# Kernel tuning notes

Hardware: AMD Instinct MI355X
Metric: run time of the kernel (lower is better)

Reference implementation:

```python
import jax, jax.numpy as jnp
import numpy as np

B, C, H, W = 16, 128, 48, 48
C4 = C // 4
N = H * W
BN_EPS = 1e-5


def conv_bn_relu(x, w, gamma, beta, mean, var):
    # 1x1 conv (no bias) as channel contraction, then eval-mode BatchNorm, then ReLU
    y = jnp.einsum('bchw,oc->bohw', x, w)
    scale = gamma / jnp.sqrt(var + BN_EPS)
    y = y * scale[None, :, None, None] + (beta - mean * scale)[None, :, None, None]
    return jax.nn.relu(y)


def setup_inputs() -> dict:
    key = jax.random.key(0)
    ks = jax.random.split(key, 16)
    inp = {
        'x_en': jax.random.normal(ks[0], (B, C, H, W), dtype=jnp.float32),
        'x_de': jax.random.normal(ks[1], (B, C, H, W), dtype=jnp.float32),
        'x_cat': jax.random.normal(ks[2], (B, 2 * C, H, W), dtype=jnp.float32),
        # Get_KQ: Conv2d(C -> C/4, 1x1, no bias) + BN(C/4) (shared for K and Q)
        'w_kq': jax.random.normal(ks[3], (C4, C), dtype=jnp.float32) * 0.05,
        'kq_gamma': jax.random.normal(ks[4], (C4,), dtype=jnp.float32) * 0.1 + 1.0,
        'kq_beta': jax.random.normal(ks[5], (C4,), dtype=jnp.float32) * 0.1,
        'kq_mean': jax.random.normal(ks[6], (C4,), dtype=jnp.float32) * 0.1,
        'kq_var': jax.random.uniform(ks[7], (C4,), dtype=jnp.float32) + 0.5,
        # Get_V: Conv2d(C -> C, 1x1, no bias) + BN(C)
        'w_v': jax.random.normal(ks[8], (C, C), dtype=jnp.float32) * 0.05,
        'v_gamma': jax.random.normal(ks[9], (C,), dtype=jnp.float32) * 0.1 + 1.0,
        'v_beta': jax.random.normal(ks[10], (C,), dtype=jnp.float32) * 0.1,
        'v_mean': jax.random.normal(ks[11], (C,), dtype=jnp.float32) * 0.1,
        'v_var': jax.random.uniform(ks[12], (C,), dtype=jnp.float32) + 0.5,
        # reduce_channels: Conv2d(2C -> C, 1x1, no bias) + BN(C)
        'w_red': jax.random.normal(ks[13], (C, 2 * C), dtype=jnp.float32) * 0.05,
        'red_gamma': jax.random.normal(ks[14], (C,), dtype=jnp.float32) * 0.1 + 1.0,
        'red_beta': jax.random.normal(ks[15], (C,), dtype=jnp.float32) * 0.1,
        'red_mean': jax.random.normal(jax.random.fold_in(key, 100), (C,), dtype=jnp.float32) * 0.1,
        'red_var': jax.random.uniform(jax.random.fold_in(key, 101), (C,), dtype=jnp.float32) + 0.5,
    }
    return inp


def reference(x_en, x_de, x_cat,
              w_kq, kq_gamma, kq_beta, kq_mean, kq_var,
              w_v, v_gamma, v_beta, v_mean, v_var,
              w_red, red_gamma, red_beta, red_mean, red_var):
    Kf = conv_bn_relu(x_en, w_kq, kq_gamma, kq_beta, kq_mean, kq_var).reshape(B, C4, N)
    Qf = conv_bn_relu(x_de, w_kq, kq_gamma, kq_beta, kq_mean, kq_var).reshape(B, C4, N)
    # KQ[b, n, m] = sum_k K[b, k, n] * Q[b, k, m]  -> [B, N, N]
    KQ = jnp.einsum('bkn,bkm->bnm', Kf, Qf)
    # GLOBAL softmax over the flattened N*N map (per batch), not per row
    A = jax.nn.softmax(KQ.reshape(B, N * N), axis=1).reshape(B, N, N)
    x = conv_bn_relu(x_cat, w_red, red_gamma, red_beta, red_mean, red_var)
    V = conv_bn_relu(x, w_v, v_gamma, v_beta, v_mean, v_var).reshape(B, C, N)
    # FeatureMap[b, c, n] = sum_m V[b, c, m] * A[b, n, m]
    feat = jnp.einsum('bcm,bnm->bcn', V, A).reshape(B, C, H, W)
    return jnp.concatenate([x, feat], axis=1)
```

## Files before the change

### kernel.cpp

```cpp
#include <hip/hip_runtime.h>
#include <math.h>

#define C    128
#define C4   32
#define NN   2304
#define BN_EPS 1e-5f
#define NEG_INF -3.402823466e38f
#define LOG2E 1.4426950408889634f

typedef short bf16x8 __attribute__((ext_vector_type(8)));
typedef float f32x4 __attribute__((ext_vector_type(4)));

#define SOFT_BARRIER() asm volatile("s_waitcnt lgkmcnt(0)\n\ts_barrier" ::: "memory")

__device__ inline unsigned short f2bf(float f) {
    unsigned int u = __float_as_uint(f);
    u += 0x7fffu + ((u >> 16) & 1u);
    return (unsigned short)(u >> 16);
}

__device__ inline unsigned int pk2bf(float a, float b) {
#if __has_builtin(__builtin_amdgcn_cvt_pk_bf16_f32)
    typedef __bf16 bf2 __attribute__((ext_vector_type(2)));
    bf2 v = __builtin_amdgcn_cvt_pk_bf16_f32(a, b);
    return __builtin_bit_cast(unsigned int, v);
#else
    unsigned int ua = __float_as_uint(a); ua += 0x7fffu + ((ua >> 16) & 1u);
    unsigned int ub = __float_as_uint(b); ub += 0x7fffu + ((ub >> 16) & 1u);
    return __builtin_amdgcn_perm(ub, ua, 0x07060302u);
#endif
}

__device__ inline float fexp2(float x) {
#if __has_builtin(__builtin_amdgcn_exp2f)
    return __builtin_amdgcn_exp2f(x);
#else
    return __expf(x * 0.69314718055994531f);
#endif
}


__global__ __launch_bounds__(256) void k_wprep(
    const float* __restrict__ wkq, const float* __restrict__ kq_g,
    const float* __restrict__ kq_b, const float* __restrict__ kq_m,
    const float* __restrict__ kq_v,
    const float* __restrict__ wv, const float* __restrict__ v_g,
    const float* __restrict__ v_b, const float* __restrict__ v_m,
    const float* __restrict__ v_v,
    const float* __restrict__ wred, const float* __restrict__ red_g,
    const float* __restrict__ red_b, const float* __restrict__ red_m,
    const float* __restrict__ red_v,
    unsigned short* __restrict__ wkq_bf, unsigned short* __restrict__ wv_bf,
    unsigned short* __restrict__ wred_bf,
    float* __restrict__ kq_sh, float* __restrict__ v_sh, float* __restrict__ red_sh)
{
    const int t = blockIdx.x * 256 + threadIdx.x;
    if (t < 4096) {
        const int o = t >> 7;
        const float sc = kq_g[o] * rsqrtf(kq_v[o] + BN_EPS);
        wkq_bf[t] = f2bf(wkq[t] * sc);
        if ((t & 127) == 0) kq_sh[o] = kq_b[o] - kq_m[o] * sc;
    } else if (t < 4096 + 16384) {
        const int e = t - 4096;
        const int o = e >> 7;
        const float sc = v_g[o] * rsqrtf(v_v[o] + BN_EPS);
        wv_bf[e] = f2bf(wv[e] * sc);
        if ((e & 127) == 0) v_sh[o] = v_b[o] - v_m[o] * sc;
    } else if (t < 4096 + 16384 + 32768) {
        const int e = t - 20480;
        const int o = e >> 8;
        const float sc = red_g[o] * rsqrtf(red_v[o] + BN_EPS);
        wred_bf[e] = f2bf(wred[e] * sc);
        if ((e & 255) == 0) red_sh[o] = red_b[o] - red_m[o] * sc;
    }
}

__global__ __launch_bounds__(256) void k_kqredv(
    const float* __restrict__ x0, const float* __restrict__ x1,
    const float* __restrict__ xcat,
    const unsigned short* __restrict__ wbf, const float* __restrict__ shift,
    unsigned short* __restrict__ Kt, unsigned short* __restrict__ Qt,
    const unsigned short* __restrict__ wred_bf, const float* __restrict__ red_sh,
    const unsigned short* __restrict__ wv_bf,  const float* __restrict__ v_sh,
    float* __restrict__ out, unsigned short* __restrict__ Vf)
{
    __shared__ __align__(16) unsigned char smem[20608];
    const int wg = blockIdx.x;
    const int tid = threadIdx.x;
    const int w = tid >> 6, lane = tid & 63;
    const int quad = lane >> 4, l16 = lane & 15;
    const int cp = tid >> 4;
    const int g  = tid & 15;

    if (wg < 768) {
        typedef unsigned short XsT[48][40];
        XsT* Xs = (XsT*)smem;
        unsigned int* Xv = (unsigned int*)(smem + 7680);

        const int b = wg / 48, n0 = (wg % 48) * 48;
        const float* xin = xcat + (size_t)b * 2 * C * NN;

        f32x4 acc[2][3];
#pragma unroll
        for (int mt = 0; mt < 2; mt++)
#pragma unroll
            for (int nt = 0; nt < 3; nt++) acc[mt][nt] = (f32x4){0.f, 0.f, 0.f, 0.f};

        float av[3], bv[3];
        {
            const float* xr = xin + (size_t)(2 * cp) * NN + n0 + g;
#pragma unroll
            for (int j = 0; j < 3; j++) { av[j] = xr[j * 16]; bv[j] = xr[NN + j * 16]; }
        }

        for (int k = 0; k < 8; ++k) {
            unsigned int uu[3];
#pragma unroll
            for (int j = 0; j < 3; j++) uu[j] = pk2bf(av[j], bv[j]);
            if (k < 7) {
                const float* xr = xin + (size_t)((k + 1) * 32 + 2 * cp) * NN + n0 + g;
#pragma unroll
                for (int j = 0; j < 3; j++) { av[j] = xr[j * 16]; bv[j] = xr[NN + j * 16]; }
            }
            unsigned int* Xw = (unsigned int*)Xs[k & 1];
#pragma unroll
            for (int j = 0; j < 3; j++)
                Xw[(j * 16 + g) * 20 + cp] = uu[j];
            SOFT_BARRIER();
            bf16x8 af[2];
#pragma unroll
            for (int mt = 0; mt < 2; mt++)
                af[mt] = *(const bf16x8*)&wred_bf[(size_t)(w * 32 + mt * 16 + l16) * (2 * C) + k * 32 + quad * 8];
#pragma unroll
            for (int nt = 0; nt < 3; nt++) {
                const bf16x8 bfr = *(const bf16x8*)&Xs[k & 1][nt * 16 + l16][quad * 8];
#pragma unroll
                for (int mt = 0; mt < 2; mt++)
                    acc[mt][nt] = __builtin_amdgcn_mfma_f32_16x16x32_bf16(af[mt], bfr, acc[mt][nt], 0, 0, 0);
            }
        }

        {
            float* ob = out + (size_t)b * (2 * C * NN);
#pragma unroll
            for (int mt = 0; mt < 2; mt++) {
                float sh[4];
#pragma unroll
                for (int r = 0; r < 4; r++) sh[r] = red_sh[w * 32 + mt * 16 + quad * 4 + r];
#pragma unroll
                for (int nt = 0; nt < 3; nt++) {
                    const int n = n0 + nt * 16 + l16;
                    float v[4];
#pragma unroll
                    for (int r = 0; r < 4; r++) {
                        const int o = w * 32 + mt * 16 + quad * 4 + r;
                        v[r] = fmaxf(acc[mt][nt][r] + sh[r], 0.f);
                        ob[(size_t)o * NN + n] = v[r];
                    }
                    const int op0 = 16 * w + mt * 8 + quad * 2;
                    Xv[(op0 + 0) * 49 + nt * 16 + l16] = pk2bf(v[0], v[1]);
                    Xv[(op0 + 1) * 49 + nt * 16 + l16] = pk2bf(v[2], v[3]);
                }
            }
        }
        SOFT_BARRIER();

        f32x4 vacc[2][3];
#pragma unroll
        for (int mt = 0; mt < 2; mt++)
#pragma unroll
            for (int nt = 0; nt < 3; nt++) vacc[mt][nt] = (f32x4){0.f, 0.f, 0.f, 0.f};

        for (int c0 = 0; c0 < C; c0 += 32) {
            bf16x8 af[2];
#pragma unroll
            for (int mt = 0; mt < 2; mt++)
                af[mt] = *(const bf16x8*)&wv_bf[(size_t)(w * 32 + mt * 16 + l16) * C + c0 + quad * 8];
#pragma unroll
            for (int nt = 0; nt < 3; nt++) {
                const int col = nt * 16 + l16;
                const int cp0 = c0 / 2 + quad * 4;
                uint4 u;
                u.x = Xv[(cp0 + 0) * 49 + col];
                u.y = Xv[(cp0 + 1) * 49 + col];
                u.z = Xv[(cp0 + 2) * 49 + col];
                u.w = Xv[(cp0 + 3) * 49 + col];
                const bf16x8 bfr = __builtin_bit_cast(bf16x8, u);
#pragma unroll
                for (int mt = 0; mt < 2; mt++)
                    vacc[mt][nt] = __builtin_amdgcn_mfma_f32_16x16x32_bf16(af[mt], bfr, vacc[mt][nt], 0, 0, 0);
            }
        }

#pragma unroll
        for (int mt = 0; mt < 2; mt++) {
            float sh[4];
#pragma unroll
            for (int r = 0; r < 4; r++) sh[r] = v_sh[w * 32 + mt * 16 + quad * 4 + r];
#pragma unroll
            for (int nt = 0; nt < 3; nt++)
#pragma unroll
                for (int r = 0; r < 4; r++) {
                    const int o = w * 32 + mt * 16 + quad * 4 + r;
                    const int n = n0 + nt * 16 + l16;
                    Vf[(((size_t)b * 72 + (n >> 5)) * 128 + o) * 32 + (n & 31)] =
                        f2bf(fmaxf(vacc[mt][nt][r] + sh[r], 0.f));
                }
        }
    } else {
        typedef unsigned short Xs2T[128][40];
        Xs2T* Xs = (Xs2T*)smem;

        const int e = wg - 768;
        const int z = e / 288;
        const int rem = e - z * 288;
        const int b = rem / 18, n0 = (rem % 18) * 128;
        const int nbase = w * 32;

        const float* xin = (z ? x1 : x0) + (size_t)b * C * NN;

        f32x4 acc[2][2];
#pragma unroll
        for (int mt = 0; mt < 2; mt++)
#pragma unroll
            for (int nt = 0; nt < 2; nt++) acc[mt][nt] = (f32x4){0.f, 0.f, 0.f, 0.f};

        float av[8], bv[8];
        {
            const float* xr = xin + (size_t)(2 * cp) * NN + n0 + g;
#pragma unroll
            for (int j = 0; j < 8; j++) { av[j] = xr[j * 16]; bv[j] = xr[NN + j * 16]; }
        }

        for (int k = 0; k < 4; ++k) {
            unsigned int uu[8];
#pragma unroll
            for (int j = 0; j < 8; j++) uu[j] = pk2bf(av[j], bv[j]);
            if (k < 3) {
                const float* xr = xin + (size_t)((k + 1) * 32 + 2 * cp) * NN + n0 + g;
#pragma unroll
                for (int j = 0; j < 8; j++) { av[j] = xr[j * 16]; bv[j] = xr[NN + j * 16]; }
            }
            unsigned int* Xw = (unsigned int*)Xs[k & 1];
#pragma unroll
            for (int j = 0; j < 8; j++)
                Xw[(j * 16 + g) * 20 + cp] = uu[j];
            SOFT_BARRIER();
            bf16x8 af[2];
#pragma unroll
            for (int mt = 0; mt < 2; mt++)
                af[mt] = *(const bf16x8*)&wbf[(size_t)(mt * 16 + l16) * C + k * 32 + quad * 8];
#pragma unroll
            for (int nt = 0; nt < 2; nt++) {
                const bf16x8 bfr = *(const bf16x8*)&Xs[k & 1][nbase + nt * 16 + l16][quad * 8];
#pragma unroll
                for (int mt = 0; mt < 2; mt++)
                    acc[mt][nt] = __builtin_amdgcn_mfma_f32_16x16x32_bf16(af[mt], bfr, acc[mt][nt], 0, 0, 0);
            }
        }

        unsigned short* ob16 = z ? Qt : Kt;
        const float osc = z ? 1.f : LOG2E;
#pragma unroll
        for (int mt = 0; mt < 2; mt++)
#pragma unroll
            for (int nt = 0; nt < 2; nt++)
#pragma unroll
                for (int r = 0; r < 4; r++) {
                    const int o = mt * 16 + quad * 4 + r;
                    const int n = n0 + nbase + nt * 16 + l16;
                    const float sh = shift[o];
                    ob16[((size_t)b * NN + n) * 32 + o] =
                        f2bf(fmaxf(acc[mt][nt][r] + sh, 0.f) * osc);
                }
    }
}

__global__ __launch_bounds__(256) void k_stats(
    const unsigned short* __restrict__ Kt, const unsigned short* __restrict__ Qt,
    float* __restrict__ bmax, float* __restrict__ bsum)
{
    const int tid = threadIdx.x;
    const int w = tid >> 6, lane = tid & 63;
    const int quad = lane >> 4, l16 = lane & 15;
    const int wg = blockIdx.x;
    const int xcd = wg & 7;
    const int slot = wg >> 3;
    const int b = xcd * 2 + slot / 324;
    const int tile = slot % 324;
    const int my = tile / 18, mx = tile % 18;
    const int n0 = mx * 128, m0 = my * 128;
    const unsigned short* Kb = Kt + (size_t)b * NN * 32;
    const unsigned short* Qb = Qt + (size_t)b * NN * 32;

    bf16x8 kf[8], qf[2];
#pragma unroll
    for (int nt = 0; nt < 8; nt++)
        kf[nt] = *(const bf16x8*)&Kb[(size_t)(n0 + nt * 16 + l16) * 32 + quad * 8];
#pragma unroll
    for (int mt = 0; mt < 2; mt++)
        qf[mt] = *(const bf16x8*)&Qb[(size_t)(m0 + w * 32 + mt * 16 + l16) * 32 + quad * 8];

    f32x4 s[16];
#pragma unroll
    for (int mt = 0; mt < 2; mt++)
#pragma unroll
        for (int nt = 0; nt < 8; nt++) {
            f32x4 z = (f32x4){0.f, 0.f, 0.f, 0.f};
            s[mt * 8 + nt] = __builtin_amdgcn_mfma_f32_16x16x32_bf16(qf[mt], kf[nt], z, 0, 0, 0);
        }

    float lmax = NEG_INF;
#pragma unroll
    for (int i = 0; i < 16; i++)
        lmax = fmaxf(lmax, fmaxf(fmaxf(s[i][0], s[i][1]), fmaxf(s[i][2], s[i][3])));
    float lsum = 0.f;
#pragma unroll
    for (int i = 0; i < 16; i++)
        lsum += fexp2(s[i][0] - lmax) + fexp2(s[i][1] - lmax) +
                fexp2(s[i][2] - lmax) + fexp2(s[i][3] - lmax);

#pragma unroll
    for (int off = 32; off > 0; off >>= 1) {
        const float omax = __shfl_xor(lmax, off);
        const float osum = __shfl_xor(lsum, off);
        const float nmax = fmaxf(lmax, omax);
        lsum = lsum * fexp2(lmax - nmax) + osum * fexp2(omax - nmax);
        lmax = nmax;
    }
    __shared__ float smax[4], ssum[4];
    if (lane == 0) { smax[w] = lmax; ssum[w] = lsum; }
    __syncthreads();
    if (tid == 0) {
        float M = smax[0], S = ssum[0];
        for (int i = 1; i < 4; i++) {
            const float nmax = fmaxf(M, smax[i]);
            S = S * fexp2(M - nmax) + ssum[i] * fexp2(smax[i] - nmax);
            M = nmax;
        }
        const int idx = (b * 18 + my) * 18 + mx;
        bmax[idx] = M;
        bsum[idx] = S;
    }
}

__global__ __launch_bounds__(256) void k_fin(
    const float* __restrict__ bmax, const float* __restrict__ bsum,
    float* __restrict__ Ms, float* __restrict__ Sinv)
{
    __shared__ float rmax[256], rsum[256];
    const int b = blockIdx.x, tid = threadIdx.x;
    float lmax = NEG_INF, lsum = 0.f;
    for (int i = tid; i < 324; i += 256) {
        const float m = bmax[b * 324 + i], s = bsum[b * 324 + i];
        const float nmax = fmaxf(lmax, m);
        lsum = lsum * fexp2(lmax - nmax) + s * fexp2(m - nmax);
        lmax = nmax;
    }
    rmax[tid] = lmax; rsum[tid] = lsum;
    __syncthreads();
    for (int st = 128; st > 0; st >>= 1) {
        if (tid < st) {
            const float m2 = rmax[tid + st], s2 = rsum[tid + st];
            const float nmax = fmaxf(rmax[tid], m2);
            rsum[tid] = rsum[tid] * fexp2(rmax[tid] - nmax) + s2 * fexp2(m2 - nmax);
            rmax[tid] = nmax;
        }
        __syncthreads();
    }
    if (tid == 0) { Ms[b] = rmax[0]; Sinv[b] = 1.f / rsum[0]; }
}

__global__ __launch_bounds__(256) void k_feat(
    const unsigned short* __restrict__ Kt, const unsigned short* __restrict__ Qt,
    const unsigned short* __restrict__ Vf, const float* __restrict__ Ms,
    const float* __restrict__ Sinv, float* __restrict__ out)
{
    __shared__ __align__(16) unsigned short Et[2][48][136];
    const int tid = threadIdx.x;
    const int w = tid >> 6, lane = tid & 63;
    const int quad = lane >> 4, l16 = lane & 15;
    const int wg = blockIdx.x;
    const int xcd = wg & 7;
    const int slot = wg >> 3;
    const int b = xcd * 2 + slot / 48;
    const int n0 = (slot % 48) * 48;
    const unsigned short* Kb = Kt + (size_t)b * NN * 32;
    const unsigned short* Qb = Qt + (size_t)b * NN * 32;
    const unsigned short* Vb = Vf + (size_t)b * 72 * 128 * 32;
    const float M = Ms[b], Si = Sinv[b];

    bf16x8 kf[3];
#pragma unroll
    for (int nt = 0; nt < 3; nt++)
        kf[nt] = *(const bf16x8*)&Kb[(size_t)(n0 + nt * 16 + l16) * 32 + quad * 8];

    f32x4 acc[2][3];
#pragma unroll
    for (int i = 0; i < 2; i++)
#pragma unroll
        for (int j = 0; j < 3; j++) acc[i][j] = (f32x4){0.f, 0.f, 0.f, 0.f};

    {
        const bf16x8 q00 = *(const bf16x8*)&Qb[(size_t)(w * 32 + l16) * 32 + quad * 8];
        const bf16x8 q01 = *(const bf16x8*)&Qb[(size_t)(w * 32 + 16 + l16) * 32 + quad * 8];
        f32x4 s0[3], s1[3];
#pragma unroll
        for (int nt = 0; nt < 3; nt++) {
            f32x4 z = (f32x4){0.f, 0.f, 0.f, 0.f};
            s0[nt] = __builtin_amdgcn_mfma_f32_16x16x32_bf16(q00, kf[nt], z, 0, 0, 0);
            s1[nt] = __builtin_amdgcn_mfma_f32_16x16x32_bf16(q01, kf[nt], z, 0, 0, 0);
        }
#pragma unroll
        for (int nt = 0; nt < 3; nt++) {
            const unsigned int a0 = pk2bf(fexp2(s0[nt][0] - M), fexp2(s0[nt][1] - M));
            const unsigned int a1 = pk2bf(fexp2(s0[nt][2] - M), fexp2(s0[nt][3] - M));
            *(uint2*)&Et[0][nt * 16 + l16][w * 32 + quad * 4] = make_uint2(a0, a1);
            const unsigned int b0 = pk2bf(fexp2(s1[nt][0] - M), fexp2(s1[nt][1] - M));
            const unsigned int b1 = pk2bf(fexp2(s1[nt][2] - M), fexp2(s1[nt][3] - M));
            *(uint2*)&Et[0][nt * 16 + l16][w * 32 + 16 + quad * 4] = make_uint2(b0, b1);
        }
    }
    bf16x8 qc0 = *(const bf16x8*)&Qb[(size_t)(128 + w * 32 + l16) * 32 + quad * 8];
    bf16x8 qc1 = *(const bf16x8*)&Qb[(size_t)(128 + w * 32 + 16 + l16) * 32 + quad * 8];
    SOFT_BARRIER();

    for (int k = 0; k < 18; ++k) {
        const int cur = k & 1;
        const int mt0 = k * 4;
        const int mq = (k + 2 < 18 ? k + 2 : 0) * 128;
        bf16x8 qn0 = *(const bf16x8*)&Qb[(size_t)(mq + w * 32 + l16) * 32 + quad * 8];
        bf16x8 qn1 = *(const bf16x8*)&Qb[(size_t)(mq + w * 32 + 16 + l16) * 32 + quad * 8];
        bf16x8 vc[2][4];
#pragma unroll
        for (int ct = 0; ct < 2; ct++)
#pragma unroll
            for (int ks = 0; ks < 4; ks++)
                vc[ct][ks] = *(const bf16x8*)&Vb[(((size_t)(mt0 + ks)) * 128 + w * 32 + ct * 16 + l16) * 32 + quad * 8];

        if (k < 17) {
            f32x4 s0[3], s1[3];
#pragma unroll
            for (int nt = 0; nt < 3; nt++) {
                f32x4 z = (f32x4){0.f, 0.f, 0.f, 0.f};
                s0[nt] = __builtin_amdgcn_mfma_f32_16x16x32_bf16(qc0, kf[nt], z, 0, 0, 0);
                s1[nt] = __builtin_amdgcn_mfma_f32_16x16x32_bf16(qc1, kf[nt], z, 0, 0, 0);
            }
#pragma unroll
            for (int nt = 0; nt < 3; nt++) {
                const unsigned int a0 = pk2bf(fexp2(s0[nt][0] - M), fexp2(s0[nt][1] - M));
                const unsigned int a1 = pk2bf(fexp2(s0[nt][2] - M), fexp2(s0[nt][3] - M));
                *(uint2*)&Et[cur ^ 1][nt * 16 + l16][w * 32 + quad * 4] = make_uint2(a0, a1);
                const unsigned int b0 = pk2bf(fexp2(s1[nt][0] - M), fexp2(s1[nt][1] - M));
                const unsigned int b1 = pk2bf(fexp2(s1[nt][2] - M), fexp2(s1[nt][3] - M));
                *(uint2*)&Et[cur ^ 1][nt * 16 + l16][w * 32 + 16 + quad * 4] = make_uint2(b0, b1);
            }
        }

        __builtin_amdgcn_s_setprio(1);
#pragma unroll
        for (int ks = 0; ks < 4; ks++) {
#pragma unroll
            for (int nt = 0; nt < 3; nt++) {
                const bf16x8 ef = *(const bf16x8*)&Et[cur][nt * 16 + l16][ks * 32 + quad * 8];
                acc[0][nt] = __builtin_amdgcn_mfma_f32_16x16x32_bf16(vc[0][ks], ef, acc[0][nt], 0, 0, 0);
                acc[1][nt] = __builtin_amdgcn_mfma_f32_16x16x32_bf16(vc[1][ks], ef, acc[1][nt], 0, 0, 0);
            }
        }
        __builtin_amdgcn_s_setprio(0);
        SOFT_BARRIER();
        qc0 = qn0;
        qc1 = qn1;
    }

    float* ob = out + (size_t)b * 2 * C * NN + (size_t)C * NN + n0;
#pragma unroll
    for (int ct = 0; ct < 2; ct++)
#pragma unroll
        for (int nt = 0; nt < 3; nt++)
#pragma unroll
            for (int r = 0; r < 4; r++) {
                const int c = w * 32 + ct * 16 + quad * 4 + r;
                ob[(size_t)c * NN + nt * 16 + l16] = acc[ct][nt][r] * Si;
            }
}

extern "C" void kernel_launch(void* const* d_in, const int* in_sizes, int n_in,
                              void* d_out, int out_size, void* d_ws, size_t ws_size,
                              hipStream_t stream)
{
    const float* x_en   = (const float*)d_in[0];
    const float* x_de   = (const float*)d_in[1];
    const float* x_cat  = (const float*)d_in[2];
    const float* w_kq   = (const float*)d_in[3];
    const float* kq_g   = (const float*)d_in[4];
    const float* kq_b   = (const float*)d_in[5];
    const float* kq_m   = (const float*)d_in[6];
    const float* kq_v   = (const float*)d_in[7];
    const float* w_v    = (const float*)d_in[8];
    const float* v_g    = (const float*)d_in[9];
    const float* v_b    = (const float*)d_in[10];
    const float* v_m    = (const float*)d_in[11];
    const float* v_v    = (const float*)d_in[12];
    const float* w_red  = (const float*)d_in[13];
    const float* red_g  = (const float*)d_in[14];
    const float* red_b  = (const float*)d_in[15];
    const float* red_m  = (const float*)d_in[16];
    const float* red_v  = (const float*)d_in[17];

    unsigned short* Kt      = (unsigned short*)d_ws;
    unsigned short* Qt      = Kt + 1179648;
    unsigned short* Vf      = Qt + 1179648;
    unsigned short* wkq_bf  = Vf + 4718592;
    unsigned short* wv_bf   = wkq_bf + 4096;
    unsigned short* wred_bf = wv_bf + 16384;
    float* bmax = (float*)(wred_bf + 32768);
    float* bsum = bmax + 16 * 324;
    float* Ms   = bsum + 16 * 324;
    float* Sinv = Ms + 16;
    float* kq_sh  = Sinv + 16;
    float* v_sh   = kq_sh + 32;
    float* red_sh = v_sh + 128;
    float* out  = (float*)d_out;

    k_wprep<<<208, 256, 0, stream>>>(
        w_kq, kq_g, kq_b, kq_m, kq_v,
        w_v, v_g, v_b, v_m, v_v,
        w_red, red_g, red_b, red_m, red_v,
        wkq_bf, wv_bf, wred_bf, kq_sh, v_sh, red_sh);

    k_kqredv<<<1344, 256, 0, stream>>>(
        x_en, x_de, x_cat, wkq_bf, kq_sh, Kt, Qt,
        wred_bf, red_sh, wv_bf, v_sh, out, Vf);

    k_stats<<<5184, 256, 0, stream>>>(Kt, Qt, bmax, bsum);
    k_fin  <<<16, 256, 0, stream>>>(bmax, bsum, Ms, Sinv);
    k_feat <<<768, 256, 0, stream>>>(Kt, Qt, Vf, Ms, Sinv, out);
}
```

Measured before the change: 220.1 us.

## Fuse softmax final reduction into feat kernel and swizzle LDS tile

Removes the separate k_fin launch. Each k_feat block now recomputes the per-batch global max and sum from the 324 partial stats itself, which trades one kernel launch and its dependency gap for some redundant reduction work in every block. The padded LDS tile for the exponentiated scores is replaced by an unpadded tile with an XOR swizzle on 16-byte chunks, meant to avoid bank conflicts while using less shared memory. The max and sum reductions in k_stats are rewritten as trees with multiple accumulators to shorten dependency chains.

```diff
diff --git a/kernel.cpp b/kernel.cpp
--- a/kernel.cpp
+++ b/kernel.cpp
@@ -310,26 +310,37 @@
             s[mt * 8 + nt] = __builtin_amdgcn_mfma_f32_16x16x32_bf16(qf[mt], kf[nt], z, 0, 0, 0);
         }
 
-    float lmax = NEG_INF;
+    float v[16];
 #pragma unroll
     for (int i = 0; i < 16; i++)
-        lmax = fmaxf(lmax, fmaxf(fmaxf(s[i][0], s[i][1]), fmaxf(s[i][2], s[i][3])));
-    float lsum = 0.f;
-#pragma unroll
-    for (int i = 0; i < 16; i++)
-        lsum += fexp2(s[i][0] - lmax) + fexp2(s[i][1] - lmax) +
-                fexp2(s[i][2] - lmax) + fexp2(s[i][3] - lmax);
+        v[i] = fmaxf(fmaxf(s[i][0], s[i][1]), fmaxf(s[i][2], s[i][3]));
+#pragma unroll
+    for (int st = 8; st > 0; st >>= 1)
+#pragma unroll
+        for (int i = 0; i < st; i++) v[i] = fmaxf(v[i], v[i + st]);
+    const float lmax = v[0];
+
+    float l0 = 0.f, l1 = 0.f, l2 = 0.f, l3 = 0.f;
+#pragma unroll
+    for (int i = 0; i < 16; i += 4) {
+        l0 += fexp2(s[i+0][0] - lmax) + fexp2(s[i+0][1] - lmax) + fexp2(s[i+0][2] - lmax) + fexp2(s[i+0][3] - lmax);
+        l1 += fexp2(s[i+1][0] - lmax) + fexp2(s[i+1][1] - lmax) + fexp2(s[i+1][2] - lmax) + fexp2(s[i+1][3] - lmax);
+        l2 += fexp2(s[i+2][0] - lmax) + fexp2(s[i+2][1] - lmax) + fexp2(s[i+2][2] - lmax) + fexp2(s[i+2][3] - lmax);
+        l3 += fexp2(s[i+3][0] - lmax) + fexp2(s[i+3][1] - lmax) + fexp2(s[i+3][2] - lmax) + fexp2(s[i+3][3] - lmax);
+    }
+    float lsum = (l0 + l1) + (l2 + l3);
+    float lm = lmax;
 
 #pragma unroll
     for (int off = 32; off > 0; off >>= 1) {
-        const float omax = __shfl_xor(lmax, off);
+        const float omax = __shfl_xor(lm, off);
         const float osum = __shfl_xor(lsum, off);
-        const float nmax = fmaxf(lmax, omax);
-        lsum = lsum * fexp2(lmax - nmax) + osum * fexp2(omax - nmax);
-        lmax = nmax;
+        const float nmax = fmaxf(lm, omax);
+        lsum = lsum * fexp2(lm - nmax) + osum * fexp2(omax - nmax);
+        lm = nmax;
     }
     __shared__ float smax[4], ssum[4];
-    if (lane == 0) { smax[w] = lmax; ssum[w] = lsum; }
+    if (lane == 0) { smax[w] = lm; ssum[w] = lsum; }
     __syncthreads();
     if (tid == 0) {
         float M = smax[0], S = ssum[0];
@@ -344,39 +355,14 @@
     }
 }
 
-__global__ __launch_bounds__(256) void k_fin(
-    const float* __restrict__ bmax, const float* __restrict__ bsum,
-    float* __restrict__ Ms, float* __restrict__ Sinv)
-{
-    __shared__ float rmax[256], rsum[256];
-    const int b = blockIdx.x, tid = threadIdx.x;
-    float lmax = NEG_INF, lsum = 0.f;
-    for (int i = tid; i < 324; i += 256) {
-        const float m = bmax[b * 324 + i], s = bsum[b * 324 + i];
-        const float nmax = fmaxf(lmax, m);
-        lsum = lsum * fexp2(lmax - nmax) + s * fexp2(m - nmax);
-        lmax = nmax;
-    }
-    rmax[tid] = lmax; rsum[tid] = lsum;
-    __syncthreads();
-    for (int st = 128; st > 0; st >>= 1) {
-        if (tid < st) {
-            const float m2 = rmax[tid + st], s2 = rsum[tid + st];
-            const float nmax = fmaxf(rmax[tid], m2);
-            rsum[tid] = rsum[tid] * fexp2(rmax[tid] - nmax) + s2 * fexp2(m2 - nmax);
-            rmax[tid] = nmax;
-        }
-        __syncthreads();
-    }
-    if (tid == 0) { Ms[b] = rmax[0]; Sinv[b] = 1.f / rsum[0]; }
-}
-
 __global__ __launch_bounds__(256) void k_feat(
     const unsigned short* __restrict__ Kt, const unsigned short* __restrict__ Qt,
-    const unsigned short* __restrict__ Vf, const float* __restrict__ Ms,
-    const float* __restrict__ Sinv, float* __restrict__ out)
+    const unsigned short* __restrict__ Vf,
+    const float* __restrict__ bmax, const float* __restrict__ bsum,
+    float* __restrict__ out)
 {
-    __shared__ __align__(16) unsigned short Et[2][48][136];
+    __shared__ __align__(16) unsigned short Et[2][48][128];
+    __shared__ float2 redw[4];
     const int tid = threadIdx.x;
     const int w = tid >> 6, lane = tid & 63;
     const int quad = lane >> 4, l16 = lane & 15;
@@ -388,7 +374,43 @@
     const unsigned short* Kb = Kt + (size_t)b * NN * 32;
     const unsigned short* Qb = Qt + (size_t)b * NN * 32;
     const unsigned short* Vb = Vf + (size_t)b * 72 * 128 * 32;
-    const float M = Ms[b], Si = Sinv[b];
+
+    float M, Si;
+    {
+        float lm = NEG_INF, ls = 0.f;
+        for (int i = tid; i < 324; i += 256) {
+            const float m = bmax[b * 324 + i], s = bsum[b * 324 + i];
+            const float nm = fmaxf(lm, m);
+            ls = ls * fexp2(lm - nm) + s * fexp2(m - nm);
+            lm = nm;
+        }
+#pragma unroll
+        for (int off = 32; off > 0; off >>= 1) {
+            const float om = __shfl_xor(lm, off);
+            const float os = __shfl_xor(ls, off);
+            const float nm = fmaxf(lm, om);
+            ls = ls * fexp2(lm - nm) + os * fexp2(om - nm);
+            lm = nm;
+        }
+        if (lane == 0) redw[w] = make_float2(lm, ls);
+        __syncthreads();
+        float Mm = redw[0].x, Ss = redw[0].y;
+#pragma unroll
+        for (int i = 1; i < 4; i++) {
+            const float m2 = redw[i].x, s2 = redw[i].y;
+            const float nm = fmaxf(Mm, m2);
+            Ss = Ss * fexp2(Mm - nm) + s2 * fexp2(m2 - nm);
+            Mm = nm;
+        }
+        M = Mm;
+        Si = 1.f / Ss;
+    }
+
+    const int aswz = l16 & 7;
+    const int wby0 = 64 * w + 8 * quad;
+    const int wof0 = ((((wby0 >> 4) ^ aswz) << 4) | (wby0 & 15));
+    const int wby1 = wby0 + 32;
+    const int wof1 = ((((wby1 >> 4) ^ aswz) << 4) | (wby1 & 15));
 
     bf16x8 kf[3];
 #pragma unroll
@@ -413,12 +435,13 @@
         }
 #pragma unroll
         for (int nt = 0; nt < 3; nt++) {
+            char* rowp = (char*)&Et[0][nt * 16 + l16][0];
             const unsigned int a0 = pk2bf(fexp2(s0[nt][0] - M), fexp2(s0[nt][1] - M));
             const unsigned int a1 = pk2bf(fexp2(s0[nt][2] - M), fexp2(s0[nt][3] - M));
-            *(uint2*)&Et[0][nt * 16 + l16][w * 32 + quad * 4] = make_uint2(a0, a1);
+            *(uint2*)(rowp + wof0) = make_uint2(a0, a1);
             const unsigned int b0 = pk2bf(fexp2(s1[nt][0] - M), fexp2(s1[nt][1] - M));
             const unsigned int b1 = pk2bf(fexp2(s1[nt][2] - M), fexp2(s1[nt][3] - M));
-            *(uint2*)&Et[0][nt * 16 + l16][w * 32 + 16 + quad * 4] = make_uint2(b0, b1);
+            *(uint2*)(rowp + wof1) = make_uint2(b0, b1);
         }
     }
     bf16x8 qc0 = *(const bf16x8*)&Qb[(size_t)(128 + w * 32 + l16) * 32 + quad * 8];
@@ -448,21 +471,24 @@
             }
 #pragma unroll
             for (int nt = 0; nt < 3; nt++) {
+                char* rowp = (char*)&Et[cur ^ 1][nt * 16 + l16][0];
                 const unsigned int a0 = pk2bf(fexp2(s0[nt][0] - M), fexp2(s0[nt][1] - M));
                 const unsigned int a1 = pk2bf(fexp2(s0[nt][2] - M), fexp2(s0[nt][3] - M));
-                *(uint2*)&Et[cur ^ 1][nt * 16 + l16][w * 32 + quad * 4] = make_uint2(a0, a1);
+                *(uint2*)(rowp + wof0) = make_uint2(a0, a1);
                 const unsigned int b0 = pk2bf(fexp2(s1[nt][0] - M), fexp2(s1[nt][1] - M));
                 const unsigned int b1 = pk2bf(fexp2(s1[nt][2] - M), fexp2(s1[nt][3] - M));
-                *(uint2*)&Et[cur ^ 1][nt * 16 + l16][w * 32 + 16 + quad * 4] = make_uint2(b0, b1);
+                *(uint2*)(rowp + wof1) = make_uint2(b0, b1);
             }
         }
 
         __builtin_amdgcn_s_setprio(1);
 #pragma unroll
         for (int ks = 0; ks < 4; ks++) {
+            const int rby = 64 * ks + 16 * quad;
+            const int rof = (((rby >> 4) ^ aswz) << 4);
 #pragma unroll
             for (int nt = 0; nt < 3; nt++) {
-                const bf16x8 ef = *(const bf16x8*)&Et[cur][nt * 16 + l16][ks * 32 + quad * 8];
+                const bf16x8 ef = *(const bf16x8*)((const char*)&Et[cur][nt * 16 + l16][0] + rof);
                 acc[0][nt] = __builtin_amdgcn_mfma_f32_16x16x32_bf16(vc[0][ks], ef, acc[0][nt], 0, 0, 0);
                 acc[1][nt] = __builtin_amdgcn_mfma_f32_16x16x32_bf16(vc[1][ks], ef, acc[1][nt], 0, 0, 0);
             }
@@ -534,6 +560,5 @@
         wred_bf, red_sh, wv_bf, v_sh, out, Vf);
 
     k_stats<<<5184, 256, 0, stream>>>(Kt, Qt, bmax, bsum);
-    k_fin  <<<16, 256, 0, stream>>>(bmax, bsum, Ms, Sinv);
-    k_feat <<<768, 256, 0, stream>>>(Kt, Qt, Vf, Ms, Sinv, out);
-}
+    k_feat <<<768, 256, 0, stream>>>(Kt, Qt, Vf, bmax, bsum, out);
+}
```

Measured after the change: 222.2 us. Within noise of the previous version (+0.9%).

## Fuse global softmax statistics into feature kernel with online max rescaling

Applied to the files above, without the earlier changes.

Removes the separate stats and finalize kernels, which recomputed the full KQ map just to get the global max and sum. The feature kernel now keeps a running block-wide max per column slice, rescales its accumulators and running sum as the max grows, and writes per-block partial max and sum. A new normalization kernel combines the 48 partials per batch and rescales the feature output in place. This adds an extra read-modify-write pass over the feature half of the output and adds a barrier and a max reduction to every iteration of the main loop.

```diff
diff --git a/kernel.cpp b/kernel.cpp
--- a/kernel.cpp
+++ b/kernel.cpp
@@ -276,107 +276,15 @@
     }
 }
 
-__global__ __launch_bounds__(256) void k_stats(
-    const unsigned short* __restrict__ Kt, const unsigned short* __restrict__ Qt,
-    float* __restrict__ bmax, float* __restrict__ bsum)
-{
-    const int tid = threadIdx.x;
-    const int w = tid >> 6, lane = tid & 63;
-    const int quad = lane >> 4, l16 = lane & 15;
-    const int wg = blockIdx.x;
-    const int xcd = wg & 7;
-    const int slot = wg >> 3;
-    const int b = xcd * 2 + slot / 324;
-    const int tile = slot % 324;
-    const int my = tile / 18, mx = tile % 18;
-    const int n0 = mx * 128, m0 = my * 128;
-    const unsigned short* Kb = Kt + (size_t)b * NN * 32;
-    const unsigned short* Qb = Qt + (size_t)b * NN * 32;
-
-    bf16x8 kf[8], qf[2];
-#pragma unroll
-    for (int nt = 0; nt < 8; nt++)
-        kf[nt] = *(const bf16x8*)&Kb[(size_t)(n0 + nt * 16 + l16) * 32 + quad * 8];
-#pragma unroll
-    for (int mt = 0; mt < 2; mt++)
-        qf[mt] = *(const bf16x8*)&Qb[(size_t)(m0 + w * 32 + mt * 16 + l16) * 32 + quad * 8];
-
-    f32x4 s[16];
-#pragma unroll
-    for (int mt = 0; mt < 2; mt++)
-#pragma unroll
-        for (int nt = 0; nt < 8; nt++) {
-            f32x4 z = (f32x4){0.f, 0.f, 0.f, 0.f};
-            s[mt * 8 + nt] = __builtin_amdgcn_mfma_f32_16x16x32_bf16(qf[mt], kf[nt], z, 0, 0, 0);
-        }
-
-    float lmax = NEG_INF;
-#pragma unroll
-    for (int i = 0; i < 16; i++)
-        lmax = fmaxf(lmax, fmaxf(fmaxf(s[i][0], s[i][1]), fmaxf(s[i][2], s[i][3])));
-    float lsum = 0.f;
-#pragma unroll
-    for (int i = 0; i < 16; i++)
-        lsum += fexp2(s[i][0] - lmax) + fexp2(s[i][1] - lmax) +
-                fexp2(s[i][2] - lmax) + fexp2(s[i][3] - lmax);
-
-#pragma unroll
-    for (int off = 32; off > 0; off >>= 1) {
-        const float omax = __shfl_xor(lmax, off);
-        const float osum = __shfl_xor(lsum, off);
-        const float nmax = fmaxf(lmax, omax);
-        lsum = lsum * fexp2(lmax - nmax) + osum * fexp2(omax - nmax);
-        lmax = nmax;
-    }
-    __shared__ float smax[4], ssum[4];
-    if (lane == 0) { smax[w] = lmax; ssum[w] = lsum; }
-    __syncthreads();
-    if (tid == 0) {
-        float M = smax[0], S = ssum[0];
-        for (int i = 1; i < 4; i++) {
-            const float nmax = fmaxf(M, smax[i]);
-            S = S * fexp2(M - nmax) + ssum[i] * fexp2(smax[i] - nmax);
-            M = nmax;
-        }
-        const int idx = (b * 18 + my) * 18 + mx;
-        bmax[idx] = M;
-        bsum[idx] = S;
-    }
-}
-
-__global__ __launch_bounds__(256) void k_fin(
-    const float* __restrict__ bmax, const float* __restrict__ bsum,
-    float* __restrict__ Ms, float* __restrict__ Sinv)
-{
-    __shared__ float rmax[256], rsum[256];
-    const int b = blockIdx.x, tid = threadIdx.x;
-    float lmax = NEG_INF, lsum = 0.f;
-    for (int i = tid; i < 324; i += 256) {
-        const float m = bmax[b * 324 + i], s = bsum[b * 324 + i];
-        const float nmax = fmaxf(lmax, m);
-        lsum = lsum * fexp2(lmax - nmax) + s * fexp2(m - nmax);
-        lmax = nmax;
-    }
-    rmax[tid] = lmax; rsum[tid] = lsum;
-    __syncthreads();
-    for (int st = 128; st > 0; st >>= 1) {
-        if (tid < st) {
-            const float m2 = rmax[tid + st], s2 = rsum[tid + st];
-            const float nmax = fmaxf(rmax[tid], m2);
-            rsum[tid] = rsum[tid] * fexp2(rmax[tid] - nmax) + s2 * fexp2(m2 - nmax);
-            rmax[tid] = nmax;
-        }
-        __syncthreads();
-    }
-    if (tid == 0) { Ms[b] = rmax[0]; Sinv[b] = 1.f / rsum[0]; }
-}
-
 __global__ __launch_bounds__(256) void k_feat(
     const unsigned short* __restrict__ Kt, const unsigned short* __restrict__ Qt,
-    const unsigned short* __restrict__ Vf, const float* __restrict__ Ms,
-    const float* __restrict__ Sinv, float* __restrict__ out)
+    const unsigned short* __restrict__ Vf,
+    float* __restrict__ partM, float* __restrict__ partS,
+    float* __restrict__ out)
 {
     __shared__ __align__(16) unsigned short Et[2][48][136];
+    __shared__ float smax[2][4];
+    __shared__ float ssum[4];
     const int tid = threadIdx.x;
     const int w = tid >> 6, lane = tid & 63;
     const int quad = lane >> 4, l16 = lane & 15;
@@ -384,11 +292,11 @@
     const int xcd = wg & 7;
     const int slot = wg >> 3;
     const int b = xcd * 2 + slot / 48;
-    const int n0 = (slot % 48) * 48;
+    const int ns = slot % 48;
+    const int n0 = ns * 48;
     const unsigned short* Kb = Kt + (size_t)b * NN * 32;
     const unsigned short* Qb = Qt + (size_t)b * NN * 32;
     const unsigned short* Vb = Vf + (size_t)b * 72 * 128 * 32;
-    const float M = Ms[b], Si = Sinv[b];
 
     bf16x8 kf[3];
 #pragma unroll
@@ -400,6 +308,9 @@
     for (int i = 0; i < 2; i++)
 #pragma unroll
         for (int j = 0; j < 3; j++) acc[i][j] = (f32x4){0.f, 0.f, 0.f, 0.f};
+
+    float S_run = 0.f;
+    float M;
 
     {
         const bf16x8 q00 = *(const bf16x8*)&Qb[(size_t)(w * 32 + l16) * 32 + quad * 8];
@@ -411,19 +322,35 @@
             s0[nt] = __builtin_amdgcn_mfma_f32_16x16x32_bf16(q00, kf[nt], z, 0, 0, 0);
             s1[nt] = __builtin_amdgcn_mfma_f32_16x16x32_bf16(q01, kf[nt], z, 0, 0, 0);
         }
+        float wm = NEG_INF;
 #pragma unroll
         for (int nt = 0; nt < 3; nt++) {
-            const unsigned int a0 = pk2bf(fexp2(s0[nt][0] - M), fexp2(s0[nt][1] - M));
-            const unsigned int a1 = pk2bf(fexp2(s0[nt][2] - M), fexp2(s0[nt][3] - M));
-            *(uint2*)&Et[0][nt * 16 + l16][w * 32 + quad * 4] = make_uint2(a0, a1);
-            const unsigned int b0 = pk2bf(fexp2(s1[nt][0] - M), fexp2(s1[nt][1] - M));
-            const unsigned int b1 = pk2bf(fexp2(s1[nt][2] - M), fexp2(s1[nt][3] - M));
-            *(uint2*)&Et[0][nt * 16 + l16][w * 32 + 16 + quad * 4] = make_uint2(b0, b1);
-        }
+            wm = fmaxf(wm, fmaxf(fmaxf(s0[nt][0], s0[nt][1]), fmaxf(s0[nt][2], s0[nt][3])));
+            wm = fmaxf(wm, fmaxf(fmaxf(s1[nt][0], s1[nt][1]), fmaxf(s1[nt][2], s1[nt][3])));
+        }
+#pragma unroll
+        for (int off = 32; off > 0; off >>= 1) wm = fmaxf(wm, __shfl_xor(wm, off));
+        if (lane == 0) smax[0][w] = wm;
+        __syncthreads();
+        M = fmaxf(fmaxf(smax[0][0], smax[0][1]), fmaxf(smax[0][2], smax[0][3]));
+        float cs = 0.f;
+#pragma unroll
+        for (int nt = 0; nt < 3; nt++) {
+            const float e0 = fexp2(s0[nt][0] - M), e1 = fexp2(s0[nt][1] - M);
+            const float e2 = fexp2(s0[nt][2] - M), e3 = fexp2(s0[nt][3] - M);
+            cs += (e0 + e1) + (e2 + e3);
+            *(uint2*)&Et[0][nt * 16 + l16][w * 32 + quad * 4] =
+                make_uint2(pk2bf(e0, e1), pk2bf(e2, e3));
+            const float f0 = fexp2(s1[nt][0] - M), f1 = fexp2(s1[nt][1] - M);
+            const float f2 = fexp2(s1[nt][2] - M), f3 = fexp2(s1[nt][3] - M);
+            cs += (f0 + f1) + (f2 + f3);
+            *(uint2*)&Et[0][nt * 16 + l16][w * 32 + 16 + quad * 4] =
+                make_uint2(pk2bf(f0, f1), pk2bf(f2, f3));
+        }
+        S_run = cs;
     }
     bf16x8 qc0 = *(const bf16x8*)&Qb[(size_t)(128 + w * 32 + l16) * 32 + quad * 8];
     bf16x8 qc1 = *(const bf16x8*)&Qb[(size_t)(128 + w * 32 + 16 + l16) * 32 + quad * 8];
-    SOFT_BARRIER();
 
     for (int k = 0; k < 18; ++k) {
         const int cur = k & 1;
@@ -438,23 +365,47 @@
             for (int ks = 0; ks < 4; ks++)
                 vc[ct][ks] = *(const bf16x8*)&Vb[(((size_t)(mt0 + ks)) * 128 + w * 32 + ct * 16 + l16) * 32 + quad * 8];
 
+        f32x4 s0[3], s1[3];
         if (k < 17) {
-            f32x4 s0[3], s1[3];
 #pragma unroll
             for (int nt = 0; nt < 3; nt++) {
                 f32x4 z = (f32x4){0.f, 0.f, 0.f, 0.f};
                 s0[nt] = __builtin_amdgcn_mfma_f32_16x16x32_bf16(qc0, kf[nt], z, 0, 0, 0);
                 s1[nt] = __builtin_amdgcn_mfma_f32_16x16x32_bf16(qc1, kf[nt], z, 0, 0, 0);
             }
+            float wm = NEG_INF;
 #pragma unroll
             for (int nt = 0; nt < 3; nt++) {
-                const unsigned int a0 = pk2bf(fexp2(s0[nt][0] - M), fexp2(s0[nt][1] - M));
-                const unsigned int a1 = pk2bf(fexp2(s0[nt][2] - M), fexp2(s0[nt][3] - M));
-                *(uint2*)&Et[cur ^ 1][nt * 16 + l16][w * 32 + quad * 4] = make_uint2(a0, a1);
-                const unsigned int b0 = pk2bf(fexp2(s1[nt][0] - M), fexp2(s1[nt][1] - M));
-                const unsigned int b1 = pk2bf(fexp2(s1[nt][2] - M), fexp2(s1[nt][3] - M));
-                *(uint2*)&Et[cur ^ 1][nt * 16 + l16][w * 32 + 16 + quad * 4] = make_uint2(b0, b1);
-            }
+                wm = fmaxf(wm, fmaxf(fmaxf(s0[nt][0], s0[nt][1]), fmaxf(s0[nt][2], s0[nt][3])));
+                wm = fmaxf(wm, fmaxf(fmaxf(s1[nt][0], s1[nt][1]), fmaxf(s1[nt][2], s1[nt][3])));
+            }
+#pragma unroll
+            for (int off = 32; off > 0; off >>= 1) wm = fmaxf(wm, __shfl_xor(wm, off));
+            if (lane == 0) smax[(k + 1) & 1][w] = wm;
+        }
+        SOFT_BARRIER();
+        float r = 1.f;
+        if (k < 17) {
+            const float cm = fmaxf(fmaxf(smax[(k + 1) & 1][0], smax[(k + 1) & 1][1]),
+                                   fmaxf(smax[(k + 1) & 1][2], smax[(k + 1) & 1][3]));
+            const float Mn = fmaxf(M, cm);
+            r = fexp2(M - Mn);
+            M = Mn;
+            float cs = 0.f;
+#pragma unroll
+            for (int nt = 0; nt < 3; nt++) {
+                const float e0 = fexp2(s0[nt][0] - M), e1 = fexp2(s0[nt][1] - M);
+                const float e2 = fexp2(s0[nt][2] - M), e3 = fexp2(s0[nt][3] - M);
+                cs += (e0 + e1) + (e2 + e3);
+                *(uint2*)&Et[cur ^ 1][nt * 16 + l16][w * 32 + quad * 4] =
+                    make_uint2(pk2bf(e0, e1), pk2bf(e2, e3));
+                const float f0 = fexp2(s1[nt][0] - M), f1 = fexp2(s1[nt][1] - M);
+                const float f2 = fexp2(s1[nt][2] - M), f3 = fexp2(s1[nt][3] - M);
+                cs += (f0 + f1) + (f2 + f3);
+                *(uint2*)&Et[cur ^ 1][nt * 16 + l16][w * 32 + 16 + quad * 4] =
+                    make_uint2(pk2bf(f0, f1), pk2bf(f2, f3));
+            }
+            S_run = S_run * r + cs;
         }
 
         __builtin_amdgcn_s_setprio(1);
@@ -468,21 +419,64 @@
             }
         }
         __builtin_amdgcn_s_setprio(0);
+#pragma unroll
+        for (int i = 0; i < 2; i++)
+#pragma unroll
+            for (int j = 0; j < 3; j++) acc[i][j] = acc[i][j] * r;
         SOFT_BARRIER();
         qc0 = qn0;
         qc1 = qn1;
     }
 
+#pragma unroll
+    for (int off = 32; off > 0; off >>= 1) S_run += __shfl_xor(S_run, off);
+    if (lane == 0) ssum[w] = S_run;
+    __syncthreads();
+    if (tid == 0) {
+        partM[b * 48 + ns] = M;
+        partS[b * 48 + ns] = (ssum[0] + ssum[1]) + (ssum[2] + ssum[3]);
+    }
+
     float* ob = out + (size_t)b * 2 * C * NN + (size_t)C * NN + n0;
 #pragma unroll
     for (int ct = 0; ct < 2; ct++)
 #pragma unroll
         for (int nt = 0; nt < 3; nt++)
 #pragma unroll
-            for (int r = 0; r < 4; r++) {
-                const int c = w * 32 + ct * 16 + quad * 4 + r;
-                ob[(size_t)c * NN + nt * 16 + l16] = acc[ct][nt][r] * Si;
-            }
+            for (int r2 = 0; r2 < 4; r2++) {
+                const int c = w * 32 + ct * 16 + quad * 4 + r2;
+                ob[(size_t)c * NN + nt * 16 + l16] = acc[ct][nt][r2];
+            }
+}
+
+__global__ __launch_bounds__(256) void k_norm(
+    const float* __restrict__ partM, const float* __restrict__ partS,
+    float* __restrict__ out)
+{
+    const int tid = threadIdx.x;
+    const int w = tid >> 6, lane = tid & 63;
+    const int wg = blockIdx.x;
+    const int xcd = wg & 7;
+    const int slot = wg >> 3;
+    const int b = xcd * 2 + slot / 48;
+    const int ns = slot % 48;
+    const int n0 = ns * 48;
+
+    const float* pM = partM + b * 48;
+    const float* pS = partS + b * 48;
+    float Mg = NEG_INF;
+#pragma unroll
+    for (int i = 0; i < 48; i++) Mg = fmaxf(Mg, pM[i]);
+    float Sg = 0.f;
+#pragma unroll
+    for (int i = 0; i < 48; i++) Sg += pS[i] * fexp2(pM[i] - Mg);
+    const float f = fexp2(pM[ns] - Mg) / Sg;
+
+    float* ob = out + (size_t)b * 2 * C * NN + (size_t)C * NN + n0;
+    if (lane < 48) {
+        for (int c = w; c < 128; c += 4)
+            ob[(size_t)c * NN + lane] *= f;
+    }
 }
 
 extern "C" void kernel_launch(void* const* d_in, const int* in_sizes, int n_in,
@@ -514,11 +508,9 @@
     unsigned short* wkq_bf  = Vf + 4718592;
     unsigned short* wv_bf   = wkq_bf + 4096;
     unsigned short* wred_bf = wv_bf + 16384;
-    float* bmax = (float*)(wred_bf + 32768);
-    float* bsum = bmax + 16 * 324;
-    float* Ms   = bsum + 16 * 324;
-    float* Sinv = Ms + 16;
-    float* kq_sh  = Sinv + 16;
+    float* partM = (float*)(wred_bf + 32768);
+    float* partS = partM + 768;
+    float* kq_sh  = partS + 768;
     float* v_sh   = kq_sh + 32;
     float* red_sh = v_sh + 128;
     float* out  = (float*)d_out;
@@ -533,7 +525,6 @@
         x_en, x_de, x_cat, wkq_bf, kq_sh, Kt, Qt,
         wred_bf, red_sh, wv_bf, v_sh, out, Vf);
 
-    k_stats<<<5184, 256, 0, stream>>>(Kt, Qt, bmax, bsum);
-    k_fin  <<<16, 256, 0, stream>>>(bmax, bsum, Ms, Sinv);
-    k_feat <<<768, 256, 0, stream>>>(Kt, Qt, Vf, Ms, Sinv, out);
-}
+    k_feat<<<768, 256, 0, stream>>>(Kt, Qt, Vf, partM, partS, out);
+    k_norm<<<768, 256, 0, stream>>>(partM, partS, out);
+}
```

Result: slower. 230.7 us (+4.8%).
